# Optimization experiments

Hardware: AMD Instinct MI355X
Metric: run time of the kernel (lower is better)

## Reference

```python
import jax, jax.numpy as jnp
import numpy as np

B, S, D = 64, 1024, 128
EPS = 1e-5

def hardswish(x):
    return x * jnp.clip(x + 3.0, 0.0, 6.0) / 6.0

def setup_inputs() -> dict:
    key = jax.random.key(0)
    k1, k2, k3 = jax.random.split(key, 3)
    x = jax.random.normal(k1, (B, S, D), dtype=jnp.float32)
    ln_w = jnp.ones((S, D), dtype=jnp.float32)
    ln_b = jnp.zeros((S, D), dtype=jnp.float32)
    # U1[i]/U2[i] rows packed into lower-triangular (S,S); init ~ N(0,1)*0.01
    W1 = jax.random.normal(k2, (S, S), dtype=jnp.float32) * 0.01
    W2 = jax.random.normal(k3, (S, S), dtype=jnp.float32) * 0.01
    return {"x": x, "ln_w": ln_w, "ln_b": ln_b, "W1": W1, "W2": W2}

def reference(x, ln_w, ln_b, W1, W2):
    # LayerNorm over the last two dims (seq_len, feature_dim) jointly
    mu = jnp.mean(x, axis=(-2, -1), keepdims=True)
    var = jnp.mean(jnp.square(x - mu), axis=(-2, -1), keepdims=True)
    h = (x - mu) * jax.lax.rsqrt(var + EPS) * ln_w + ln_b
    # causal (lower-triangular) time mixing: u[:, t] = sum_{s<=t} W1[t, s] * h[:, s]
    mask = jnp.tril(jnp.ones((S, S), dtype=x.dtype))
    u = hardswish(jnp.einsum('ts,bsd->btd', W1 * mask, h))
    v = jnp.einsum('ts,bsd->btd', W2 * mask, u)
    return x + v
```

## Files before the change

### kernel.cpp

```cpp
#include <hip/hip_runtime.h>
#include <hip/hip_bf16.h>

#define NB 64
#define S_ 1024
#define D_ 128

typedef __attribute__((ext_vector_type(8))) short bf16x8;
typedef __attribute__((ext_vector_type(4))) float f32x4;
typedef __attribute__((ext_vector_type(4))) unsigned int u32x4;


__device__ __forceinline__ unsigned short f2bf(float f) {
  __hip_bfloat16 h = __float2bfloat16(f);
  return __builtin_bit_cast(unsigned short, h);
}

__device__ __forceinline__ void async_copy16(const void* g, void* l) {
  __builtin_amdgcn_global_load_lds(
      (const __attribute__((address_space(1))) unsigned int*)g,
      (__attribute__((address_space(3))) unsigned int*)l, 16, 0, 0);
}

__device__ __forceinline__ void store16_dev(void* p, bf16x8 v) {
  u32x4 d = __builtin_bit_cast(u32x4, v);
  asm volatile("global_store_dwordx4 %0, %1, off sc1" ::"v"(p), "v"(d)
               : "memory");
}

__device__ __forceinline__ void spin_mask(unsigned* p, unsigned need) {
  if (threadIdx.x == 0) {
    int guard = 0;
    while ((__hip_atomic_load(p, __ATOMIC_RELAXED, __HIP_MEMORY_SCOPE_AGENT) &
            need) != need) {
      __builtin_amdgcn_s_sleep(4);
      if (++guard > 400000) break;
    }
  }
  __syncthreads();
  asm volatile("" ::: "memory");
}

__device__ __forceinline__ void spin_cnt(unsigned* p, unsigned need) {
  if (threadIdx.x == 0) {
    int guard = 0;
    while (__hip_atomic_load(p, __ATOMIC_RELAXED, __HIP_MEMORY_SCOPE_AGENT) <
           need) {
      __builtin_amdgcn_s_sleep(4);
      if (++guard > 400000) break;
    }
  }
  __syncthreads();
  asm volatile("" ::: "memory");
}

__device__ __forceinline__ void publish_bit(unsigned* p, unsigned bit) {
  asm volatile("s_waitcnt vmcnt(0)" ::: "memory");
  __syncthreads();
  if (threadIdx.x == 0)
    __hip_atomic_fetch_or(p, bit, __ATOMIC_RELAXED, __HIP_MEMORY_SCOPE_AGENT);
}

__global__ __launch_bounds__(256) void init_stats(unsigned* __restrict__ c) {
#pragma unroll
  for (int i = 0; i < 8; ++i) c[threadIdx.x + i * 256] = 0u;
}

template <bool HSWISH>
__device__ __forceinline__ void gemm_phase(
    unsigned short* ldsA, const int b, const int mt,
    const unsigned short* __restrict__ Af, const unsigned short* __restrict__ Bf,
    unsigned short* __restrict__ Uf, const float* __restrict__ Xres,
    float* __restrict__ Out) {
  const int t = threadIdx.x;
  const int wave = t >> 6, lane = t & 63;
  const int quad = lane >> 4, l16 = lane & 15;
  const int row0 = mt * 64;

  const int cend = 2 * (mt + 1);
  const int npan = (cend + 7) >> 3;

  const unsigned short* Ab = Af + (size_t)mt * 4 * 32 * 512;
  const unsigned short* Bb = Bf + (size_t)b * (D_ * S_);

  f32x4 acc[4][2] = {};
  bf16x8 Bp[4][2];
#pragma unroll
  for (int g = 0; g < 4; ++g) {
    const int gg = (g < cend) ? g : 0;
#pragma unroll
    for (int jj = 0; jj < 2; ++jj)
      Bp[g][jj] = *(const bf16x8*)(Bb + ((size_t)(wave * 2 + jj) * 32 + gg) * 512 + lane * 8);
  }

  for (int p = 0; p < npan; ++p) {
    if (p) __syncthreads();
    const int rem = cend - p * 8;
#pragma unroll
    for (int jc = 0; jc < 8; ++jc) {
      const int flat16 = jc * 256 + t;
      const int iw = flat16 >> 9;
      const int cc = (flat16 >> 6) & 7;
      const int li = flat16 & 63;
      if (cc < rem)
        async_copy16(Ab + ((size_t)iw * 32 + p * 8 + cc) * 512 + li * 8,
                     ldsA + flat16 * 8);
    }
    __syncthreads();
#pragma unroll
    for (int c = 0; c < 8; ++c) {
      const int g = p * 8 + c;
      if (g < cend) {
        bf16x8 af[4];
#pragma unroll
        for (int i = 0; i < 4; ++i)
          af[i] = *(const bf16x8*)(ldsA + i * 4096 + c * 512 + lane * 8);
        __builtin_amdgcn_s_setprio(1);
#pragma unroll
        for (int i = 0; i < 4; ++i)
#pragma unroll
          for (int jj = 0; jj < 2; ++jj)
            acc[i][jj] = __builtin_amdgcn_mfma_f32_16x16x32_bf16(
                af[i], Bp[c & 3][jj], acc[i][jj], 0, 0, 0);
        __builtin_amdgcn_s_setprio(0);
        const int gn = (g + 4 < cend) ? (g + 4) : 0;
#pragma unroll
        for (int jj = 0; jj < 2; ++jj)
          Bp[c & 3][jj] = *(const bf16x8*)(
              Bb + ((size_t)(wave * 2 + jj) * 32 + gn) * 512 + lane * 8);
      }
    }
  }

  if (HSWISH) {
    __syncthreads();
    unsigned short* ldsT = ldsA;
#pragma unroll
    for (int i = 0; i < 4; ++i)
#pragma unroll
      for (int jj = 0; jj < 2; ++jj) {
        ushort4 pk;
        float v0 = acc[i][jj][0], v1 = acc[i][jj][1], v2 = acc[i][jj][2], v3 = acc[i][jj][3];
        pk.x = f2bf(v0 * fminf(fmaxf(v0 + 3.f, 0.f), 6.f) * (1.f / 6.f));
        pk.y = f2bf(v1 * fminf(fmaxf(v1 + 3.f, 0.f), 6.f) * (1.f / 6.f));
        pk.z = f2bf(v2 * fminf(fmaxf(v2 + 3.f, 0.f), 6.f) * (1.f / 6.f));
        pk.w = f2bf(v3 * fminf(fmaxf(v3 + 3.f, 0.f), 6.f) * (1.f / 6.f));
        const int n = wave * 32 + jj * 16 + l16;
        const int m0 = i * 16 + quad * 4;
        *(ushort4*)(ldsT + n * 72 + m0) = pk;
      }
    __syncthreads();
    unsigned short* gU = Uf + (size_t)b * (D_ * S_);
#pragma unroll
    for (int ff = 0; ff < 4; ++ff) {
      const int f = wave * 4 + ff;
      const int p2 = f >> 1, cl = f & 1;
      const int d = p2 * 16 + l16;
      const int tb = cl * 32 + quad * 8;
      bf16x8 v = *(const bf16x8*)(ldsT + d * 72 + tb);
      store16_dev(gU + ((size_t)p2 * 32 + mt * 2 + cl) * 512 + lane * 8, v);
    }
  } else {
    float* gO = Out + (size_t)b * S_ * D_;
    const float* gX = Xres + (size_t)b * S_ * D_;
#pragma unroll
    for (int i = 0; i < 4; ++i) {
      const int mrow0 = row0 + i * 16 + quad * 4;
#pragma unroll
      for (int jj = 0; jj < 2; ++jj) {
        const int col = wave * 32 + jj * 16 + l16;
#pragma unroll
        for (int r = 0; r < 4; ++r) {
          const int addr = (mrow0 + r) * D_ + col;
          gO[addr] = gX[addr] + acc[i][jj][r];
        }
      }
    }
  }
}

__global__ __launch_bounds__(256, 4) void mega_kernel(
    const float* __restrict__ x, const float* __restrict__ ln_w,
    const float* __restrict__ ln_b, const float* __restrict__ W1,
    const float* __restrict__ W2, float* __restrict__ stats,
    unsigned short* __restrict__ W1f, unsigned short* __restrict__ W2f,
    unsigned short* __restrict__ hTf, unsigned short* __restrict__ uTf,
    float* __restrict__ out) {
  __shared__ __align__(16) unsigned short smem[16384];

  const int bi = blockIdx.x;
  const int xcd = bi & 7;
  const int slot = bi >> 3;
  const int b = xcd * 8 + (slot & 7);
  const int j = slot >> 3;
  const int mt = (j < 8) ? j : (j ^ 3);

  const int t = threadIdx.x;
  const int wave = t >> 6, lane = t & 63;
  const int quad = lane >> 4, l16 = lane & 15;

  float* sb = stats + (size_t)b * 32;
  unsigned* cntp = (unsigned*)sb + 2;
  unsigned* hmp = (unsigned*)sb + 4;
  unsigned* ump = (unsigned*)sb + 6;
  unsigned* wcnt = (unsigned*)stats + 16;

  float2* w4 = (float2*)(smem + 8448);
  float* mr = (float*)(smem + 8464);

  const float4* xb = (const float4*)(x + ((size_t)b * S_ + mt * 64) * D_);
  float4 xv[8];
  {
    float s = 0.f, q = 0.f;
#pragma unroll
    for (int i = 0; i < 8; ++i) {
      float4 v = xb[i * 256 + t];
      xv[i] = v;
      s += v.x + v.y + v.z + v.w;
      q += v.x * v.x + v.y * v.y + v.z * v.z + v.w * v.w;
    }
#pragma unroll
    for (int o = 32; o > 0; o >>= 1) {
      s += __shfl_down(s, o, 64);
      q += __shfl_down(q, o, 64);
    }
    if (lane == 0) w4[wave] = make_float2(s, q);
  }
  __syncthreads();
  if (t == 0) {
    float ss = 0.f, qq = 0.f;
#pragma unroll
    for (int i = 0; i < 4; ++i) { ss += w4[i].x; qq += w4[i].y; }
    float o1 = __hip_atomic_fetch_add(sb + 0, ss, __ATOMIC_RELAXED,
                                      __HIP_MEMORY_SCOPE_AGENT);
    float o2 = __hip_atomic_fetch_add(sb + 1, qq, __ATOMIC_RELAXED,
                                      __HIP_MEMORY_SCOPE_AGENT);
    asm volatile("" ::"v"(o1), "v"(o2));
    __hip_atomic_fetch_add(cntp, 1u, __ATOMIC_RELAXED,
                           __HIP_MEMORY_SCOPE_AGENT);
  }

  {
    const int u = bi * 4 + wave;
    const int f = u & 2047;
    const int p = f >> 5, c = f & 31;
    const int r = p * 16 + l16;
    const int k0 = c * 32 + quad * 8;
    const float* wsrc = ((u >> 11) ? W2 : W1) + (size_t)r * 1024 + k0;
    float4 a0 = ((const float4*)wsrc)[0];
    float4 a1 = ((const float4*)wsrc)[1];
    float av[8] = {a0.x, a0.y, a0.z, a0.w, a1.x, a1.y, a1.z, a1.w};
    bf16x8 o;
#pragma unroll
    for (int jj = 0; jj < 8; ++jj)
      o[jj] = (short)f2bf((k0 + jj <= r) ? av[jj] : 0.f);
    unsigned short* dstp = ((u >> 11) ? W2f : W1f) +
                           ((size_t)p * 32 + c) * 512 + lane * 8;
    store16_dev(dstp, o);
  }
  asm volatile("s_waitcnt vmcnt(0)" ::: "memory");
  __syncthreads();
  if (t == 0) {
    __hip_atomic_fetch_add(wcnt, 1u, __ATOMIC_RELAXED,
                           __HIP_MEMORY_SCOPE_AGENT);
    int guard = 0;
    while (__hip_atomic_load(cntp, __ATOMIC_RELAXED,
                             __HIP_MEMORY_SCOPE_AGENT) < 16u) {
      __builtin_amdgcn_s_sleep(4);
      if (++guard > 400000) break;
    }
    float s1 = __hip_atomic_load(sb + 0, __ATOMIC_RELAXED,
                                 __HIP_MEMORY_SCOPE_AGENT);
    float s2 = __hip_atomic_load(sb + 1, __ATOMIC_RELAXED,
                                 __HIP_MEMORY_SCOPE_AGENT);
    const float inv = 1.0f / (S_ * D_);
    const float mu = s1 * inv;
    mr[0] = mu;
    mr[1] = rsqrtf(s2 * inv - mu * mu + 1e-5f);
  }
  __syncthreads();
  const float mu = mr[0];
  const float rs = mr[1];

  {
    unsigned short* lds = smem;
    const float4* wb = (const float4*)(ln_w + (size_t)(mt * 64) * D_);
    const float4* bv4 = (const float4*)(ln_b + (size_t)(mt * 64) * D_);
#pragma unroll
    for (int r = 0; r < 8; ++r) {
      const int f = r * 256 + t;
      const int srow = f >> 5;
      const int c4 = f & 31;
      float4 wv = wb[f];
      float4 bvv = bv4[f];
      ushort4 o;
      o.x = f2bf((xv[r].x - mu) * rs * wv.x + bvv.x);
      o.y = f2bf((xv[r].y - mu) * rs * wv.y + bvv.y);
      o.z = f2bf((xv[r].z - mu) * rs * wv.z + bvv.z);
      o.w = f2bf((xv[r].w - mu) * rs * wv.w + bvv.w);
      *(ushort4*)(lds + srow * 132 + c4 * 4) = o;
    }
    __syncthreads();
    unsigned short* outp = hTf + (size_t)b * (D_ * S_);
    const int cg0 = mt * 2;
#pragma unroll
    for (int ff = 0; ff < 4; ++ff) {
      const int f = wave * 4 + ff;
      const int p = f >> 1, cl = f & 1;
      const int d = p * 16 + l16;
      const int sbase = cl * 32 + quad * 8;
      bf16x8 v;
#pragma unroll
      for (int jj = 0; jj < 8; ++jj)
        v[jj] = (short)lds[(sbase + jj) * 132 + d];
      store16_dev(outp + ((size_t)p * 32 + cg0 + cl) * 512 + lane * 8, v);
    }
  }
  publish_bit(hmp, 1u << mt);

  spin_cnt(wcnt, 1024);
  spin_mask(hmp, (2u << mt) - 1);
  gemm_phase<true>(smem, b, mt, W1f, hTf, uTf, nullptr, nullptr);
  publish_bit(ump, 1u << mt);

  const int mt2 = 15 - mt;
  spin_mask(ump, (2u << mt2) - 1);
  gemm_phase<false>(smem, b, mt2, W2f, uTf, nullptr, x, out);
}

extern "C" void kernel_launch(void* const* d_in, const int* in_sizes, int n_in,
                              void* d_out, int out_size, void* d_ws, size_t ws_size,
                              hipStream_t stream) {
  const float* x = (const float*)d_in[0];
  const float* ln_w = (const float*)d_in[1];
  const float* ln_b = (const float*)d_in[2];
  const float* W1 = (const float*)d_in[3];
  const float* W2 = (const float*)d_in[4];
  float* out = (float*)d_out;

  char* ws = (char*)d_ws;
  float* stats = (float*)ws;
  unsigned short* W1f = (unsigned short*)(ws + 16384);
  unsigned short* W2f = W1f + (size_t)S_ * S_;
  unsigned short* hTf = W2f + (size_t)S_ * S_;
  unsigned short* uTf = hTf + (size_t)NB * D_ * S_;

  init_stats<<<1, 256, 0, stream>>>((unsigned*)stats);
  mega_kernel<<<1024, 256, 0, stream>>>(x, ln_w, ln_b, W1, W2, stats,
                                        W1f, W2f, hTf, uTf, out);
}
```

Before: 146.9 us.

## Split each GEMM tile across two column halves, doubling blocks and occupancy

The persistent mega-kernel now launches 2048 blocks instead of 1024. Each (batch, row-tile) pair is split into two column halves, each with half the accumulators and LDS. LayerNorm stats and h production go to the nh=0 blocks, and the nh=1 blocks take over the weight bf16 conversion. Phase 2 now reuses the same row tile rather than the mirrored 15-mt tile, with a separate u-ready mask per half, and spin sleeps are shortened. The goal is higher occupancy and more parallelism to hide the dependency spin-waits, at the cost of more blocks spinning and less B-operand reuse per block.

```diff
diff --git a/kernel.cpp b/kernel.cpp
--- a/kernel.cpp
+++ b/kernel.cpp
@@ -32,8 +32,8 @@
     int guard = 0;
     while ((__hip_atomic_load(p, __ATOMIC_RELAXED, __HIP_MEMORY_SCOPE_AGENT) &
             need) != need) {
-      __builtin_amdgcn_s_sleep(4);
-      if (++guard > 400000) break;
+      __builtin_amdgcn_s_sleep(1);
+      if (++guard > 2000000) break;
     }
   }
   __syncthreads();
@@ -45,8 +45,8 @@
     int guard = 0;
     while (__hip_atomic_load(p, __ATOMIC_RELAXED, __HIP_MEMORY_SCOPE_AGENT) <
            need) {
-      __builtin_amdgcn_s_sleep(4);
-      if (++guard > 400000) break;
+      __builtin_amdgcn_s_sleep(1);
+      if (++guard > 2000000) break;
     }
   }
   __syncthreads();
@@ -60,74 +60,58 @@
     __hip_atomic_fetch_or(p, bit, __ATOMIC_RELAXED, __HIP_MEMORY_SCOPE_AGENT);
 }
 
-__global__ __launch_bounds__(256) void init_stats(unsigned* __restrict__ c) {
-#pragma unroll
-  for (int i = 0; i < 8; ++i) c[threadIdx.x + i * 256] = 0u;
-}
-
 template <bool HSWISH>
 __device__ __forceinline__ void gemm_phase(
-    unsigned short* ldsA, const int b, const int mt,
+    unsigned short* ldsA, const int b, const int mt, const int nh,
     const unsigned short* __restrict__ Af, const unsigned short* __restrict__ Bf,
     unsigned short* __restrict__ Uf, const float* __restrict__ Xres,
     float* __restrict__ Out) {
   const int t = threadIdx.x;
   const int wave = t >> 6, lane = t & 63;
   const int quad = lane >> 4, l16 = lane & 15;
-  const int row0 = mt * 64;
 
   const int cend = 2 * (mt + 1);
-  const int npan = (cend + 7) >> 3;
+  const int nhp = (cend + 3) >> 2;
 
   const unsigned short* Ab = Af + (size_t)mt * 4 * 32 * 512;
   const unsigned short* Bb = Bf + (size_t)b * (D_ * S_);
-
-  f32x4 acc[4][2] = {};
-  bf16x8 Bp[4][2];
+  const int pcol = nh * 4 + wave;
+
+  f32x4 acc[4] = {};
+  bf16x8 Bp[4];
 #pragma unroll
   for (int g = 0; g < 4; ++g) {
     const int gg = (g < cend) ? g : 0;
-#pragma unroll
-    for (int jj = 0; jj < 2; ++jj)
-      Bp[g][jj] = *(const bf16x8*)(Bb + ((size_t)(wave * 2 + jj) * 32 + gg) * 512 + lane * 8);
-  }
-
-  for (int p = 0; p < npan; ++p) {
-    if (p) __syncthreads();
-    const int rem = cend - p * 8;
-#pragma unroll
-    for (int jc = 0; jc < 8; ++jc) {
-      const int flat16 = jc * 256 + t;
-      const int iw = flat16 >> 9;
-      const int cc = (flat16 >> 6) & 7;
-      const int li = flat16 & 63;
-      if (cc < rem)
-        async_copy16(Ab + ((size_t)iw * 32 + p * 8 + cc) * 512 + li * 8,
-                     ldsA + flat16 * 8);
-    }
-    __syncthreads();
-#pragma unroll
-    for (int c = 0; c < 8; ++c) {
-      const int g = p * 8 + c;
+    Bp[g] = *(const bf16x8*)(Bb + ((size_t)pcol * 32 + gg) * 512 + lane * 8);
+  }
+
+  for (int hp = 0; hp < nhp; ++hp) {
+    __syncthreads();
+    const int rem = cend - hp * 4;
+    if (wave < rem) {
+#pragma unroll
+      for (int jc = 0; jc < 4; ++jc)
+        async_copy16(Ab + ((size_t)jc * 32 + hp * 4 + wave) * 512 + lane * 8,
+                     ldsA + ((size_t)jc * 256 + t) * 8);
+    }
+    __syncthreads();
+#pragma unroll
+    for (int c = 0; c < 4; ++c) {
+      const int g = hp * 4 + c;
       if (g < cend) {
         bf16x8 af[4];
 #pragma unroll
         for (int i = 0; i < 4; ++i)
-          af[i] = *(const bf16x8*)(ldsA + i * 4096 + c * 512 + lane * 8);
+          af[i] = *(const bf16x8*)(ldsA + i * 2048 + c * 512 + lane * 8);
         __builtin_amdgcn_s_setprio(1);
 #pragma unroll
         for (int i = 0; i < 4; ++i)
-#pragma unroll
-          for (int jj = 0; jj < 2; ++jj)
-            acc[i][jj] = __builtin_amdgcn_mfma_f32_16x16x32_bf16(
-                af[i], Bp[c & 3][jj], acc[i][jj], 0, 0, 0);
+          acc[i] = __builtin_amdgcn_mfma_f32_16x16x32_bf16(af[i], Bp[c],
+                                                           acc[i], 0, 0, 0);
         __builtin_amdgcn_s_setprio(0);
-        const int gn = (g + 4 < cend) ? (g + 4) : 0;
-#pragma unroll
-        for (int jj = 0; jj < 2; ++jj)
-          Bp[c & 3][jj] = *(const bf16x8*)(
-              Bb + ((size_t)(wave * 2 + jj) * 32 + gn) * 512 + lane * 8);
-      }
+      }
+      const int gn = (g + 4 < cend) ? (g + 4) : 0;
+      Bp[c] = *(const bf16x8*)(Bb + ((size_t)pcol * 32 + gn) * 512 + lane * 8);
     }
   }
 
@@ -135,64 +119,62 @@
     __syncthreads();
     unsigned short* ldsT = ldsA;
 #pragma unroll
-    for (int i = 0; i < 4; ++i)
-#pragma unroll
-      for (int jj = 0; jj < 2; ++jj) {
-        ushort4 pk;
-        float v0 = acc[i][jj][0], v1 = acc[i][jj][1], v2 = acc[i][jj][2], v3 = acc[i][jj][3];
-        pk.x = f2bf(v0 * fminf(fmaxf(v0 + 3.f, 0.f), 6.f) * (1.f / 6.f));
-        pk.y = f2bf(v1 * fminf(fmaxf(v1 + 3.f, 0.f), 6.f) * (1.f / 6.f));
-        pk.z = f2bf(v2 * fminf(fmaxf(v2 + 3.f, 0.f), 6.f) * (1.f / 6.f));
-        pk.w = f2bf(v3 * fminf(fmaxf(v3 + 3.f, 0.f), 6.f) * (1.f / 6.f));
-        const int n = wave * 32 + jj * 16 + l16;
-        const int m0 = i * 16 + quad * 4;
-        *(ushort4*)(ldsT + n * 72 + m0) = pk;
-      }
+    for (int i = 0; i < 4; ++i) {
+      ushort4 pk;
+      float v0 = acc[i][0], v1 = acc[i][1], v2 = acc[i][2], v3 = acc[i][3];
+      pk.x = f2bf(v0 * fminf(fmaxf(v0 + 3.f, 0.f), 6.f) * (1.f / 6.f));
+      pk.y = f2bf(v1 * fminf(fmaxf(v1 + 3.f, 0.f), 6.f) * (1.f / 6.f));
+      pk.z = f2bf(v2 * fminf(fmaxf(v2 + 3.f, 0.f), 6.f) * (1.f / 6.f));
+      pk.w = f2bf(v3 * fminf(fmaxf(v3 + 3.f, 0.f), 6.f) * (1.f / 6.f));
+      const int n = wave * 16 + l16;
+      const int m0 = i * 16 + quad * 4;
+      *(ushort4*)(ldsT + n * 68 + m0) = pk;
+    }
     __syncthreads();
     unsigned short* gU = Uf + (size_t)b * (D_ * S_);
 #pragma unroll
-    for (int ff = 0; ff < 4; ++ff) {
-      const int f = wave * 4 + ff;
-      const int p2 = f >> 1, cl = f & 1;
-      const int d = p2 * 16 + l16;
+    for (int ff = 0; ff < 2; ++ff) {
+      const int cl = ff;
+      const int d = wave * 16 + l16;
       const int tb = cl * 32 + quad * 8;
-      bf16x8 v = *(const bf16x8*)(ldsT + d * 72 + tb);
-      store16_dev(gU + ((size_t)p2 * 32 + mt * 2 + cl) * 512 + lane * 8, v);
+      bf16x8 v = *(const bf16x8*)(ldsT + d * 68 + tb);
+      store16_dev(gU + ((size_t)(nh * 4 + wave) * 32 + mt * 2 + cl) * 512 +
+                      lane * 8,
+                  v);
     }
   } else {
     float* gO = Out + (size_t)b * S_ * D_;
     const float* gX = Xres + (size_t)b * S_ * D_;
+    const int col = nh * 64 + wave * 16 + l16;
 #pragma unroll
     for (int i = 0; i < 4; ++i) {
-      const int mrow0 = row0 + i * 16 + quad * 4;
-#pragma unroll
-      for (int jj = 0; jj < 2; ++jj) {
-        const int col = wave * 32 + jj * 16 + l16;
-#pragma unroll
-        for (int r = 0; r < 4; ++r) {
-          const int addr = (mrow0 + r) * D_ + col;
-          gO[addr] = gX[addr] + acc[i][jj][r];
-        }
-      }
-    }
-  }
-}
-
-__global__ __launch_bounds__(256, 4) void mega_kernel(
+      const int mrow0 = mt * 64 + i * 16 + quad * 4;
+#pragma unroll
+      for (int r = 0; r < 4; ++r) {
+        const int addr = (mrow0 + r) * D_ + col;
+        gO[addr] = gX[addr] + acc[i][r];
+      }
+    }
+  }
+}
+
+__global__ __launch_bounds__(256, 8) void mega_kernel(
     const float* __restrict__ x, const float* __restrict__ ln_w,
     const float* __restrict__ ln_b, const float* __restrict__ W1,
     const float* __restrict__ W2, float* __restrict__ stats,
     unsigned short* __restrict__ W1f, unsigned short* __restrict__ W2f,
     unsigned short* __restrict__ hTf, unsigned short* __restrict__ uTf,
     float* __restrict__ out) {
-  __shared__ __align__(16) unsigned short smem[16384];
+  __shared__ __align__(16) unsigned short smem[8480];
 
   const int bi = blockIdx.x;
   const int xcd = bi & 7;
   const int slot = bi >> 3;
   const int b = xcd * 8 + (slot & 7);
-  const int j = slot >> 3;
+  const int r = slot >> 3;
+  const int j = r & 15;
   const int mt = (j < 8) ? j : (j ^ 3);
+  const int nh = r >> 4;
 
   const int t = threadIdx.x;
   const int wave = t >> 6, lane = t & 63;
@@ -201,130 +183,129 @@
   float* sb = stats + (size_t)b * 32;
   unsigned* cntp = (unsigned*)sb + 2;
   unsigned* hmp = (unsigned*)sb + 4;
-  unsigned* ump = (unsigned*)sb + 6;
+  unsigned* ump0 = (unsigned*)sb + 6;
+  unsigned* ump1 = (unsigned*)sb + 8;
   unsigned* wcnt = (unsigned*)stats + 16;
 
-  float2* w4 = (float2*)(smem + 8448);
-  float* mr = (float*)(smem + 8464);
-
-  const float4* xb = (const float4*)(x + ((size_t)b * S_ + mt * 64) * D_);
-  float4 xv[8];
-  {
-    float s = 0.f, q = 0.f;
-#pragma unroll
-    for (int i = 0; i < 8; ++i) {
-      float4 v = xb[i * 256 + t];
-      xv[i] = v;
-      s += v.x + v.y + v.z + v.w;
-      q += v.x * v.x + v.y * v.y + v.z * v.z + v.w * v.w;
-    }
-#pragma unroll
-    for (int o = 32; o > 0; o >>= 1) {
-      s += __shfl_down(s, o, 64);
-      q += __shfl_down(q, o, 64);
-    }
-    if (lane == 0) w4[wave] = make_float2(s, q);
-  }
-  __syncthreads();
-  if (t == 0) {
-    float ss = 0.f, qq = 0.f;
-#pragma unroll
-    for (int i = 0; i < 4; ++i) { ss += w4[i].x; qq += w4[i].y; }
-    float o1 = __hip_atomic_fetch_add(sb + 0, ss, __ATOMIC_RELAXED,
-                                      __HIP_MEMORY_SCOPE_AGENT);
-    float o2 = __hip_atomic_fetch_add(sb + 1, qq, __ATOMIC_RELAXED,
-                                      __HIP_MEMORY_SCOPE_AGENT);
-    asm volatile("" ::"v"(o1), "v"(o2));
-    __hip_atomic_fetch_add(cntp, 1u, __ATOMIC_RELAXED,
-                           __HIP_MEMORY_SCOPE_AGENT);
-  }
-
-  {
-    const int u = bi * 4 + wave;
+  if (nh == 0) {
+    float2* w4 = (float2*)(smem + 8448);
+    float* mr = (float*)(smem + 8464);
+    const float4* xb = (const float4*)(x + ((size_t)b * S_ + mt * 64) * D_);
+    {
+      float s = 0.f, q = 0.f;
+#pragma unroll
+      for (int i = 0; i < 8; ++i) {
+        float4 v = xb[i * 256 + t];
+        s += v.x + v.y + v.z + v.w;
+        q += v.x * v.x + v.y * v.y + v.z * v.z + v.w * v.w;
+      }
+#pragma unroll
+      for (int o = 32; o > 0; o >>= 1) {
+        s += __shfl_down(s, o, 64);
+        q += __shfl_down(q, o, 64);
+      }
+      if (lane == 0) w4[wave] = make_float2(s, q);
+    }
+    __syncthreads();
+    if (t == 0) {
+      float ss = 0.f, qq = 0.f;
+#pragma unroll
+      for (int i = 0; i < 4; ++i) { ss += w4[i].x; qq += w4[i].y; }
+      float o1 = __hip_atomic_fetch_add(sb + 0, ss, __ATOMIC_RELAXED,
+                                        __HIP_MEMORY_SCOPE_AGENT);
+      float o2 = __hip_atomic_fetch_add(sb + 1, qq, __ATOMIC_RELAXED,
+                                        __HIP_MEMORY_SCOPE_AGENT);
+      asm volatile("" ::"v"(o1), "v"(o2));
+      __hip_atomic_fetch_add(cntp, 1u, __ATOMIC_RELAXED,
+                             __HIP_MEMORY_SCOPE_AGENT);
+      int guard = 0;
+      while (__hip_atomic_load(cntp, __ATOMIC_RELAXED,
+                               __HIP_MEMORY_SCOPE_AGENT) < 16u) {
+        __builtin_amdgcn_s_sleep(1);
+        if (++guard > 2000000) break;
+      }
+      float s1 = __hip_atomic_load(sb + 0, __ATOMIC_RELAXED,
+                                   __HIP_MEMORY_SCOPE_AGENT);
+      float s2 = __hip_atomic_load(sb + 1, __ATOMIC_RELAXED,
+                                   __HIP_MEMORY_SCOPE_AGENT);
+      const float inv = 1.0f / (S_ * D_);
+      const float mu = s1 * inv;
+      mr[0] = mu;
+      mr[1] = rsqrtf(s2 * inv - mu * mu + 1e-5f);
+    }
+    __syncthreads();
+    const float mu = mr[0];
+    const float rs = mr[1];
+
+    {
+      unsigned short* lds = smem;
+      const float4* wb = (const float4*)(ln_w + (size_t)(mt * 64) * D_);
+      const float4* bv4 = (const float4*)(ln_b + (size_t)(mt * 64) * D_);
+#pragma unroll
+      for (int rr = 0; rr < 8; ++rr) {
+        const int f = rr * 256 + t;
+        const int srow = f >> 5;
+        const int c4 = f & 31;
+        float4 xv = xb[f];
+        float4 wv = wb[f];
+        float4 bvv = bv4[f];
+        ushort4 o;
+        o.x = f2bf((xv.x - mu) * rs * wv.x + bvv.x);
+        o.y = f2bf((xv.y - mu) * rs * wv.y + bvv.y);
+        o.z = f2bf((xv.z - mu) * rs * wv.z + bvv.z);
+        o.w = f2bf((xv.w - mu) * rs * wv.w + bvv.w);
+        *(ushort4*)(lds + srow * 132 + c4 * 4) = o;
+      }
+      __syncthreads();
+      unsigned short* outp = hTf + (size_t)b * (D_ * S_);
+      const int cg0 = mt * 2;
+#pragma unroll
+      for (int ff = 0; ff < 4; ++ff) {
+        const int f = wave * 4 + ff;
+        const int p = f >> 1, cl = f & 1;
+        const int d = p * 16 + l16;
+        const int sbase = cl * 32 + quad * 8;
+        bf16x8 v;
+#pragma unroll
+        for (int jj = 0; jj < 8; ++jj)
+          v[jj] = (short)lds[(sbase + jj) * 132 + d];
+        store16_dev(outp + ((size_t)p * 32 + cg0 + cl) * 512 + lane * 8, v);
+      }
+    }
+    publish_bit(hmp, 1u << mt);
+  } else {
+    const int idx = xcd * 128 + (slot & 7) * 16 + (r - 16);
+    const int u = idx * 4 + wave;
     const int f = u & 2047;
     const int p = f >> 5, c = f & 31;
-    const int r = p * 16 + l16;
+    const int rr = p * 16 + l16;
     const int k0 = c * 32 + quad * 8;
-    const float* wsrc = ((u >> 11) ? W2 : W1) + (size_t)r * 1024 + k0;
+    const float* wsrc = ((u >> 11) ? W2 : W1) + (size_t)rr * 1024 + k0;
     float4 a0 = ((const float4*)wsrc)[0];
     float4 a1 = ((const float4*)wsrc)[1];
     float av[8] = {a0.x, a0.y, a0.z, a0.w, a1.x, a1.y, a1.z, a1.w};
     bf16x8 o;
 #pragma unroll
     for (int jj = 0; jj < 8; ++jj)
-      o[jj] = (short)f2bf((k0 + jj <= r) ? av[jj] : 0.f);
+      o[jj] = (short)f2bf((k0 + jj <= rr) ? av[jj] : 0.f);
     unsigned short* dstp = ((u >> 11) ? W2f : W1f) +
                            ((size_t)p * 32 + c) * 512 + lane * 8;
     store16_dev(dstp, o);
-  }
-  asm volatile("s_waitcnt vmcnt(0)" ::: "memory");
-  __syncthreads();
-  if (t == 0) {
-    __hip_atomic_fetch_add(wcnt, 1u, __ATOMIC_RELAXED,
-                           __HIP_MEMORY_SCOPE_AGENT);
-    int guard = 0;
-    while (__hip_atomic_load(cntp, __ATOMIC_RELAXED,
-                             __HIP_MEMORY_SCOPE_AGENT) < 16u) {
-      __builtin_amdgcn_s_sleep(4);
-      if (++guard > 400000) break;
-    }
-    float s1 = __hip_atomic_load(sb + 0, __ATOMIC_RELAXED,
-                                 __HIP_MEMORY_SCOPE_AGENT);
-    float s2 = __hip_atomic_load(sb + 1, __ATOMIC_RELAXED,
-                                 __HIP_MEMORY_SCOPE_AGENT);
-    const float inv = 1.0f / (S_ * D_);
-    const float mu = s1 * inv;
-    mr[0] = mu;
-    mr[1] = rsqrtf(s2 * inv - mu * mu + 1e-5f);
-  }
-  __syncthreads();
-  const float mu = mr[0];
-  const float rs = mr[1];
-
-  {
-    unsigned short* lds = smem;
-    const float4* wb = (const float4*)(ln_w + (size_t)(mt * 64) * D_);
-    const float4* bv4 = (const float4*)(ln_b + (size_t)(mt * 64) * D_);
-#pragma unroll
-    for (int r = 0; r < 8; ++r) {
-      const int f = r * 256 + t;
-      const int srow = f >> 5;
-      const int c4 = f & 31;
-      float4 wv = wb[f];
-      float4 bvv = bv4[f];
-      ushort4 o;
-      o.x = f2bf((xv[r].x - mu) * rs * wv.x + bvv.x);
-      o.y = f2bf((xv[r].y - mu) * rs * wv.y + bvv.y);
-      o.z = f2bf((xv[r].z - mu) * rs * wv.z + bvv.z);
-      o.w = f2bf((xv[r].w - mu) * rs * wv.w + bvv.w);
-      *(ushort4*)(lds + srow * 132 + c4 * 4) = o;
-    }
-    __syncthreads();
-    unsigned short* outp = hTf + (size_t)b * (D_ * S_);
-    const int cg0 = mt * 2;
-#pragma unroll
-    for (int ff = 0; ff < 4; ++ff) {
-      const int f = wave * 4 + ff;
-      const int p = f >> 1, cl = f & 1;
-      const int d = p * 16 + l16;
-      const int sbase = cl * 32 + quad * 8;
-      bf16x8 v;
-#pragma unroll
-      for (int jj = 0; jj < 8; ++jj)
-        v[jj] = (short)lds[(sbase + jj) * 132 + d];
-      store16_dev(outp + ((size_t)p * 32 + cg0 + cl) * 512 + lane * 8, v);
-    }
-  }
-  publish_bit(hmp, 1u << mt);
+    asm volatile("s_waitcnt vmcnt(0)" ::: "memory");
+    __syncthreads();
+    if (t == 0)
+      __hip_atomic_fetch_add(wcnt, 1u, __ATOMIC_RELAXED,
+                             __HIP_MEMORY_SCOPE_AGENT);
+  }
 
   spin_cnt(wcnt, 1024);
   spin_mask(hmp, (2u << mt) - 1);
-  gemm_phase<true>(smem, b, mt, W1f, hTf, uTf, nullptr, nullptr);
-  publish_bit(ump, 1u << mt);
-
-  const int mt2 = 15 - mt;
-  spin_mask(ump, (2u << mt2) - 1);
-  gemm_phase<false>(smem, b, mt2, W2f, uTf, nullptr, x, out);
+  gemm_phase<true>(smem, b, mt, nh, W1f, hTf, uTf, nullptr, nullptr);
+  publish_bit(nh ? ump1 : ump0, 1u << mt);
+
+  spin_mask(ump0, (2u << mt) - 1);
+  spin_mask(ump1, (2u << mt) - 1);
+  gemm_phase<false>(smem, b, mt, nh, W2f, uTf, nullptr, x, out);
 }
 
 extern "C" void kernel_launch(void* const* d_in, const int* in_sizes, int n_in,
@@ -344,7 +325,7 @@
   unsigned short* hTf = W2f + (size_t)S_ * S_;
   unsigned short* uTf = hTf + (size_t)NB * D_ * S_;
 
-  init_stats<<<1, 256, 0, stream>>>((unsigned*)stats);
-  mega_kernel<<<1024, 256, 0, stream>>>(x, ln_w, ln_b, W1, W2, stats,
+  hipMemsetAsync(stats, 0, 8192, stream);
+  mega_kernel<<<2048, 256, 0, stream>>>(x, ln_w, ln_b, W1, W2, stats,
                                         W1f, W2f, hTf, uTf, out);
 }
```

Result: slower. 186.6 us (+27.0%).
